# Kernel optimization log

Measured on AMD Instinct MI355X. Metric: run time of the kernel, lower is better.

## Reference

```python
import jax, jax.numpy as jnp
import numpy as np
from jax import lax

VOCAB, EMBED, CELL, LABELS = 32000, 128, 256, 128
B, T = 64, 256
N_LAYERS = 8


def _lstm_layer(x, mask, Wi, Wh, b, reverse):
    """Keras-semantics masked LSTM. x:[B,T,D], mask:[B,T] bool.
    If reverse (go_backwards=True): process reversed seq and return the
    REVERSED output sequence (Keras does NOT flip it back).
    Masked steps: carry h,c and emit previous h (Keras rnn mask behavior).
    Gate order i,f,c,o as in Keras kernels."""
    if reverse:
        x = x[:, ::-1]
        mask = mask[:, ::-1]
    Bs = x.shape[0]
    H = Wh.shape[0]
    xW = jnp.einsum('btd,dg->btg', x, Wi) + b  # [B,T,4H] precomputed input proj

    def step(carry, inp):
        h, c = carry
        g, m = inp  # g:[B,4H], m:[B]
        z = g + h @ Wh
        i, f, cb, o = jnp.split(z, 4, axis=-1)
        i = jax.nn.sigmoid(i)
        f = jax.nn.sigmoid(f)
        o = jax.nn.sigmoid(o)
        c_new = f * c + i * jnp.tanh(cb)
        h_new = o * jnp.tanh(c_new)
        m_ = m[:, None]
        h = jnp.where(m_, h_new, h)
        c = jnp.where(m_, c_new, c)
        return (h, c), h

    h0 = jnp.zeros((Bs, H), x.dtype)
    _, ys = lax.scan(step, (h0, h0), (xW.transpose(1, 0, 2), mask.T))
    return ys.transpose(1, 0, 2)  # [B,T,H], in processing order (no re-flip)


def setup_inputs() -> dict:
    key = jax.random.key(0)
    ks = jax.random.split(key, 9)
    word_ids = jax.random.randint(ks[0], (B, T), 0, VOCAB, dtype=jnp.int32)
    predicate_ids = jax.random.randint(ks[1], (B, T), 0, 2, dtype=jnp.int32)
    emb1 = jax.random.normal(ks[2], (VOCAB, EMBED), jnp.float32) * 0.1
    # binary feature embedding init: row0 zeros, row1 ones (as in source)
    emb2 = jnp.vstack([jnp.zeros((1, EMBED)), jnp.ones((1, EMBED))]).astype(jnp.float32)
    s = 0.05
    Wis = jax.random.normal(ks[3], (N_LAYERS, CELL, 4 * CELL), jnp.float32) * s  # layer0 in-dim 2*EMBED==CELL
    Whs = jax.random.normal(ks[4], (N_LAYERS, CELL, 4 * CELL), jnp.float32) * s
    bs = jnp.zeros((N_LAYERS, 4 * CELL), jnp.float32)
    bs = bs.at[:, CELL:2 * CELL].set(1.0)  # unit_forget_bias
    Wd = jax.random.normal(ks[5], (CELL, LABELS), jnp.float32) * s
    bd = jnp.zeros((LABELS,), jnp.float32)
    return {'word_ids': word_ids, 'predicate_ids': predicate_ids,
            'emb1': emb1, 'emb2': emb2, 'Wis': Wis, 'Whs': Whs, 'bs': bs,
            'Wd': Wd, 'bd': bd}


def reference(word_ids, predicate_ids, emb1, emb2, Wis, Whs, bs, Wd, bd):
    mask = word_ids != 0  # mask_zero semantics of embedding1
    encoded0 = jnp.concatenate([emb1[word_ids], emb2[predicate_ids]], axis=2)  # [B,T,2E]
    outs = []
    for i in range(N_LAYERS):
        if i == 0:
            inp = encoded0
        elif i == 1:
            inp = outs[0]
        else:
            inp = outs[i - 2] + outs[i - 1]
        outs.append(_lstm_layer(inp, mask, Wis[i], Whs[i], bs[i], reverse=(i % 2 == 1)))
    encoded_2d = (outs[6] + outs[7]).reshape(-1, CELL)  # [B*T, CELL]
    return jax.nn.softmax(encoded_2d @ Wd + bd, axis=-1)
```

## Files before the change

### kernel.cpp

```cpp
#include <hip/hip_runtime.h>


typedef _Float16 f16;
typedef _Float16 f16x8 __attribute__((ext_vector_type(8)));
typedef _Float16 f16x4 __attribute__((ext_vector_type(4)));
typedef float    f32x4 __attribute__((ext_vector_type(4)));

#define DEVI static __device__ __forceinline__

DEVI float fast_sigmoid(float x) {
  return __builtin_amdgcn_rcpf(1.f + __builtin_amdgcn_exp2f(-1.44269504f * x));
}
DEVI float fast_tanh(float x) {
  return 1.f - 2.f * __builtin_amdgcn_rcpf(1.f + __builtin_amdgcn_exp2f(2.88539008f * x));
}
DEVI int ntg_of(int w, int j2) { return ((j2 >> 1) << 4) + 2 * w + (j2 & 1); }

__global__ void pack_frags(const float* __restrict__ src, f16* __restrict__ dst, int nct) {
  const int idx  = blockIdx.x * 256 + threadIdx.x;
  const int lane = idx & 63;
  const int f    = idx >> 6;
  const int nt   = f % nct;
  const int g2   = f / nct;
  const int kk   = g2 & 7;
  const int L    = g2 >> 3;
  const int ncols = nct * 16;
  const float* s = src + (size_t)(L * 256 + kk * 32 + (lane >> 4) * 8) * ncols + nt * 16 + (lane & 15);
  f16x8 v;
#pragma unroll
  for (int e = 0; e < 8; ++e) v[e] = (f16)s[(size_t)e * ncols];
  *(f16x8*)(dst + (size_t)idx * 8) = v;
}

__global__ void embed_k(const int* __restrict__ wid, const int* __restrict__ pid,
                        const float* __restrict__ emb1, const float* __restrict__ emb2,
                        f16* __restrict__ X) {
  const int r = blockIdx.x;
  const int d = threadIdx.x;
  const int wv = wid[r], pv = pid[r];
  X[r * 256 + d]       = (f16)emb1[wv * 128 + d];
  X[r * 256 + 128 + d] = (f16)emb2[pv * 128 + d];
}

__global__ void make_input(const f16* __restrict__ a, const f16* __restrict__ b,
                           f16* __restrict__ X) {
  const size_t q = ((size_t)blockIdx.x * 256 + threadIdx.x) * 8;
  const f16x8 va = *(const f16x8*)(a + q);
  const f16x8 vb = *(const f16x8*)(b + q);
  *(f16x8*)(X + q) = va + vb;
}

__global__ __launch_bounds__(512, 2) void gemm_xw(const f16* __restrict__ X,
                                                  const f16* __restrict__ wipf,
                                                  const float* __restrict__ bias,
                                                  f16* __restrict__ xWp) {
  extern __shared__ char smem[];
  const int tid = threadIdx.x, lane = tid & 63, w = tid >> 6;
  const int nb = blockIdx.x, mb = blockIdx.y;
  const char* xbase = (const char*)X + (size_t)mb * 128 * 512;
#pragma unroll
  for (int i = 0; i < 8; ++i) {
    const int row = i * 16 + (tid >> 5);
    const int c16 = tid & 31;
    const uint4 v = *(const uint4*)(xbase + row * 512 + c16 * 16);
    *(uint4*)(smem + row * 512 + ((c16 ^ (row & 7)) << 4)) = v;
  }
  __syncthreads();

  const int mh = w >> 2, nw = w & 3;
  const char* wipf_c = (const char*)wipf;
  const float vb0 = bias[nb * 128 + nw * 32 + (lane & 15)];
  const float vb1 = bias[nb * 128 + nw * 32 + 16 + (lane & 15)];
  f32x4 acc[4][2] = {};
#pragma unroll
  for (int kk = 0; kk < 8; ++kk) {
    const f16x8 b0 = *(const f16x8*)(wipf_c + ((size_t)(kk * 64 + nb * 8 + nw * 2 + 0) << 10) + (lane << 4));
    const f16x8 b1 = *(const f16x8*)(wipf_c + ((size_t)(kk * 64 + nb * 8 + nw * 2 + 1) << 10) + (lane << 4));
#pragma unroll
    for (int m2 = 0; m2 < 4; ++m2) {
      const int row = mh * 64 + m2 * 16 + (lane & 15);
      const f16x8 a = *(const f16x8*)(smem + row * 512 + (((kk * 4 + (lane >> 4)) ^ (row & 7)) << 4));
      acc[m2][0] = __builtin_amdgcn_mfma_f32_16x16x32_f16(a, b0, acc[m2][0], 0, 0, 0);
      acc[m2][1] = __builtin_amdgcn_mfma_f32_16x16x32_f16(a, b1, acc[m2][1], 0, 0, 0);
    }
  }
#pragma unroll
  for (int m2 = 0; m2 < 4; ++m2)
#pragma unroll
    for (int n2 = 0; n2 < 2; ++n2)
#pragma unroll
      for (int j = 0; j < 4; ++j) {
        const int r   = mb * 128 + mh * 64 + m2 * 16 + (lane >> 4) * 4 + j;
        const int col = nb * 128 + nw * 32 + n2 * 16 + (lane & 15);
        xWp[(size_t)r * 1024 + (col & 255) * 4 + (col >> 8)] =
            (f16)(acc[m2][n2][j] + (n2 ? vb1 : vb0));
      }
}

__global__ __launch_bounds__(512, 2) void lstm_layer(
    const f16*  __restrict__ xWp,
    const int*  __restrict__ wid,
    const f16*  __restrict__ whp,
    f16* __restrict__ out,
    int reverse) {
  extern __shared__ char smem[];
  f16*      hbuf   = (f16*)(smem + 131072);
  unsigned* mask16 = (unsigned*)(smem + 147968);
  const int tid  = threadIdx.x;
  const int lane = tid & 63, w = tid >> 6;
  const int g    = blockIdx.x;
  const int r0   = lane & 15, rg = lane >> 4;
  const int ct0  = 2 * w;
  const char* whp_c = (const char*)whp;

  {
    const char* src = whp_c + (4 << 16);
#pragma unroll
    for (int i = 0; i < 16; ++i) {
      const int off = i * 8192 + tid * 16;
      *(uint4*)(smem + off) = *(const uint4*)(src + off);
    }
  }
  for (int i = tid; i < 2 * 16 * 264; i += 512) hbuf[i] = (f16)0.f;
  if (tid < 256) {
    unsigned m = 0;
#pragma unroll
    for (int j = 0; j < 16; ++j)
      m |= (wid[((g * 16 + j) << 8) + tid] != 0) ? (1u << j) : 0u;
    mask16[tid] = m;
  }

  f16x8 regB[32];
#pragma unroll
  for (int kk = 0; kk < 4; ++kk)
#pragma unroll
    for (int j2 = 0; j2 < 8; ++j2)
      regB[kk * 8 + j2] = *(const f16x8*)(whp_c + ((size_t)(kk * 64 + ntg_of(w, j2)) << 10) + (lane << 4));

  f16x8 sb6[8], sb7[8];
#pragma unroll
  for (int j2 = 0; j2 < 8; ++j2) {
    sb6[j2] = *(const f16x8*)(whp_c + ((size_t)(6 * 64 + ntg_of(w, j2)) << 10) + (lane << 4));
    sb7[j2] = *(const f16x8*)(whp_c + ((size_t)(7 * 64 + ntg_of(w, j2)) << 10) + (lane << 4));
  }

  float c[8], hreg[8];
#pragma unroll
  for (int i = 0; i < 8; ++i) { c[i] = 0.f; hreg[i] = 0.f; }

  __syncthreads();

#pragma unroll 1
  for (int k = 0; k < 256; ++k) {
    const int t_in = reverse ? (255 - k) : k;
    const f16* hc = hbuf + (k & 1) * 4224;
    f16*       hn = hbuf + ((k & 1) ^ 1) * 4224;

    f16x4 xwc[2][4];
#pragma unroll
    for (int p = 0; p < 2; ++p)
#pragma unroll
      for (int j = 0; j < 4; ++j)
        xwc[p][j] = *(const f16x4*)(xWp + (size_t)(((g * 16 + rg * 4 + j) << 8) + t_in) * 1024
                                    + ((ct0 + p) * 16 + r0) * 4);

    f32x4 acc[8] = {};
#pragma unroll
    for (int kk = 0; kk < 4; ++kk) {
      const f16x8 a = *(const f16x8*)&hc[r0 * 264 + kk * 32 + rg * 8];
#pragma unroll
      for (int j2 = 0; j2 < 8; ++j2)
        acc[j2] = __builtin_amdgcn_mfma_f32_16x16x32_f16(a, regB[kk * 8 + j2], acc[j2], 0, 0, 0);
    }

#pragma unroll
    for (int kk = 4; kk < 6; ++kk) {
      const f16x8 a = *(const f16x8*)&hc[r0 * 264 + kk * 32 + rg * 8];
#pragma unroll
      for (int j2 = 0; j2 < 8; ++j2) {
        const f16x8 b8 = *(const f16x8*)(smem + ((size_t)((kk - 4) * 64 + ntg_of(w, j2)) << 10) + (lane << 4));
        acc[j2] = __builtin_amdgcn_mfma_f32_16x16x32_f16(a, b8, acc[j2], 0, 0, 0);
      }
    }

    {
      const f16x8 a6 = *(const f16x8*)&hc[r0 * 264 + 6 * 32 + rg * 8];
#pragma unroll
      for (int j2 = 0; j2 < 8; ++j2)
        acc[j2] = __builtin_amdgcn_mfma_f32_16x16x32_f16(a6, sb6[j2], acc[j2], 0, 0, 0);
      const f16x8 a7 = *(const f16x8*)&hc[r0 * 264 + 7 * 32 + rg * 8];
#pragma unroll
      for (int j2 = 0; j2 < 8; ++j2)
        acc[j2] = __builtin_amdgcn_mfma_f32_16x16x32_f16(a7, sb7[j2], acc[j2], 0, 0, 0);
    }

    __builtin_amdgcn_sched_barrier(0);
#pragma unroll
    for (int j2 = 0; j2 < 8; ++j2) {
      sb6[j2] = *(const f16x8*)(whp_c + ((size_t)(6 * 64 + ntg_of(w, j2)) << 10) + (lane << 4));
      sb7[j2] = *(const f16x8*)(whp_c + ((size_t)(7 * 64 + ntg_of(w, j2)) << 10) + (lane << 4));
    }
    __builtin_amdgcn_sched_barrier(0);

    const unsigned mw = mask16[t_in];
#pragma unroll
    for (int p = 0; p < 2; ++p) {
#pragma unroll
      for (int j = 0; j < 4; ++j) {
        const int idx = p * 4 + j;
        const float zi = acc[0 + p][j] + (float)xwc[p][j][0];
        const float zf = acc[2 + p][j] + (float)xwc[p][j][1];
        const float zc = acc[4 + p][j] + (float)xwc[p][j][2];
        const float zo = acc[6 + p][j] + (float)xwc[p][j][3];
        const float ig = fast_sigmoid(zi);
        const float fg = fast_sigmoid(zf);
        const float og = fast_sigmoid(zo);
        const float cb = fast_tanh(zc);
        const float cn = fg * c[idx] + ig * cb;
        const float hv_ = og * fast_tanh(cn);
        const bool  m  = ((mw >> (rg * 4 + j)) & 1u) != 0u;
        c[idx]    = m ? cn : c[idx];
        hreg[idx] = m ? hv_ : hreg[idx];
      }
    }

#pragma unroll
    for (int p = 0; p < 2; ++p)
#pragma unroll
      for (int j = 0; j < 4; ++j) {
        const f16 hv = (f16)hreg[p * 4 + j];
        hn[(rg * 4 + j) * 264 + (ct0 + p) * 16 + r0] = hv;
        out[((size_t)((g * 16 + rg * 4 + j) << 8) + k) * 256 + (ct0 + p) * 16 + r0] = hv;
      }

    __builtin_amdgcn_sched_barrier(0);
    asm volatile("s_waitcnt lgkmcnt(0)\n\ts_barrier" ::: "memory");
    __builtin_amdgcn_sched_barrier(0);
  }
}

__global__ __launch_bounds__(512, 2) void final_k(const f16* __restrict__ o0,
                                                  const f16* __restrict__ o1,
                                                  const f16* __restrict__ wdpf,
                                                  const float* __restrict__ bd,
                                                  float* __restrict__ outp) {
  const int tid = threadIdx.x, lane = tid & 63, w = tid >> 6;
  const int rbase = blockIdx.x * 128 + w * 16;
  const char* wdpf_c = (const char*)wdpf;

  f32x4 acc[8] = {};
#pragma unroll
  for (int kk = 0; kk < 8; ++kk) {
    const int r  = rbase + (lane & 15);
    const int k0 = kk * 32 + (lane >> 4) * 8;
    const f16x8 x = *(const f16x8*)(o0 + (size_t)r * 256 + k0);
    const f16x8 y = *(const f16x8*)(o1 + (size_t)r * 256 + k0);
    const f16x8 a = x + y;
#pragma unroll
    for (int nt = 0; nt < 8; ++nt) {
      const f16x8 b = *(const f16x8*)(wdpf_c + ((size_t)(kk * 8 + nt) << 10) + (lane << 4));
      acc[nt] = __builtin_amdgcn_mfma_f32_16x16x32_f16(a, b, acc[nt], 0, 0, 0);
    }
  }

  float vb[8];
#pragma unroll
  for (int nt = 0; nt < 8; ++nt) vb[nt] = bd[nt * 16 + (lane & 15)];

#pragma unroll
  for (int j = 0; j < 4; ++j) {
    float v[8];
#pragma unroll
    for (int nt = 0; nt < 8; ++nt) v[nt] = acc[nt][j] + vb[nt];
    float mx = v[0];
#pragma unroll
    for (int nt = 1; nt < 8; ++nt) mx = fmaxf(mx, v[nt]);
#pragma unroll
    for (int m = 1; m < 16; m <<= 1) mx = fmaxf(mx, __shfl_xor(mx, m, 64));
    float s = 0.f;
#pragma unroll
    for (int nt = 0; nt < 8; ++nt) {
      v[nt] = __builtin_amdgcn_exp2f(1.44269504f * (v[nt] - mx));
      s += v[nt];
    }
#pragma unroll
    for (int m = 1; m < 16; m <<= 1) s += __shfl_xor(s, m, 64);
    const float rs = __builtin_amdgcn_rcpf(s);
    const int r = rbase + (lane >> 4) * 4 + j;
#pragma unroll
    for (int nt = 0; nt < 8; ++nt)
      outp[(size_t)r * 128 + nt * 16 + (lane & 15)] = v[nt] * rs;
  }
}

extern "C" void kernel_launch(void* const* d_in, const int* in_sizes, int n_in,
                              void* d_out, int out_size, void* d_ws, size_t ws_size,
                              hipStream_t stream) {
  const int*   wid  = (const int*)d_in[0];
  const int*   pid  = (const int*)d_in[1];
  const float* emb1 = (const float*)d_in[2];
  const float* emb2 = (const float*)d_in[3];
  const float* Wis  = (const float*)d_in[4];
  const float* Whs  = (const float*)d_in[5];
  const float* bs   = (const float*)d_in[6];
  const float* Wd   = (const float*)d_in[7];
  const float* bd   = (const float*)d_in[8];

  char* ws = (char*)d_ws;
  f16* Whp  = (f16*)(ws + 0);
  f16* Wipf = (f16*)(ws + 4194304);
  f16* Wdpf = (f16*)(ws + 8388608);
  f16* X    = (f16*)(ws + 8454144);
  f16* xWp  = (f16*)(ws + 16842752);
  f16* o0   = (f16*)(ws + 50397184);
  f16* o1   = (f16*)(ws + 58785792);

  hipFuncSetAttribute((const void*)gemm_xw,    hipFuncAttributeMaxDynamicSharedMemorySize, 65536);
  hipFuncSetAttribute((const void*)lstm_layer, hipFuncAttributeMaxDynamicSharedMemorySize, 148992);

  pack_frags<<<1024, 256, 0, stream>>>(Whs, Whp, 64);
  pack_frags<<<1024, 256, 0, stream>>>(Wis, Wipf, 64);
  pack_frags<<<16,   256, 0, stream>>>(Wd,  Wdpf, 8);
  embed_k<<<16384, 128, 0, stream>>>(wid, pid, emb1, emb2, X);

  f16* obuf[2] = {o0, o1};
  for (int L = 0; L < 8; ++L) {
    const f16* xin = X;
    if (L == 1) {
      xin = o0;
    } else if (L >= 2) {
      make_input<<<2048, 256, 0, stream>>>(obuf[L & 1], obuf[(L - 1) & 1], X);
    }
    gemm_xw<<<dim3(8, 128), 512, 65536, stream>>>(xin, Wipf + (size_t)L * 262144,
                                                  bs + L * 1024, xWp);
    lstm_layer<<<4, 512, 148992, stream>>>(xWp, wid, Whp + (size_t)L * 262144,
                                           obuf[L & 1], L & 1);
  }
  final_k<<<128, 512, 0, stream>>>(o0, o1, Wdpf, bd, (float*)d_out);
}
```

Measured before the change: 10.47 ms.

## Split LSTM recurrence across eight blocks with eight batch rows each

The recurrent LSTM kernel now runs 8 workgroups of 8 batch rows instead of 4 of 16, doubling the number of CUs working on the serial time loop. MFMA tiles still compute 16 rows, so half the rows are padding. Gate pre-activations are staged through an LDS z-buffer in two halves so each thread handles two columns of one row. This adds three extra barriers per timestep and uses a single h buffer instead of double buffering, trading more synchronisation and wasted MFMA work for more parallelism per step.

```diff
diff --git a/kernel.cpp b/kernel.cpp
--- a/kernel.cpp
+++ b/kernel.cpp
@@ -5,6 +5,7 @@
 typedef _Float16 f16x8 __attribute__((ext_vector_type(8)));
 typedef _Float16 f16x4 __attribute__((ext_vector_type(4)));
 typedef float    f32x4 __attribute__((ext_vector_type(4)));
+typedef float    f32x2 __attribute__((ext_vector_type(2)));
 
 #define DEVI static __device__ __forceinline__
 
@@ -104,14 +105,17 @@
     f16* __restrict__ out,
     int reverse) {
   extern __shared__ char smem[];
-  f16*      hbuf   = (f16*)(smem + 131072);
-  unsigned* mask16 = (unsigned*)(smem + 147968);
+  f16*      hbuf  = (f16*)(smem + 131072);
+  float*    zbuf  = (float*)(smem + 131072 + 8448);
+  unsigned* mask8 = (unsigned*)(smem + 131072 + 8448 + 16384);
   const int tid  = threadIdx.x;
   const int lane = tid & 63, w = tid >> 6;
   const int g    = blockIdx.x;
   const int r0   = lane & 15, rg = lane >> 4;
-  const int ct0  = 2 * w;
   const char* whp_c = (const char*)whp;
+  const int gr = w;
+  const int gc = lane * 2;
+  const size_t growbase = ((size_t)(g * 8 + gr)) << 8;
 
   {
     const char* src = whp_c + (4 << 16);
@@ -121,13 +125,13 @@
       *(uint4*)(smem + off) = *(const uint4*)(src + off);
     }
   }
-  for (int i = tid; i < 2 * 16 * 264; i += 512) hbuf[i] = (f16)0.f;
+  for (int i = tid; i < 16 * 264; i += 512) hbuf[i] = (f16)0.f;
   if (tid < 256) {
     unsigned m = 0;
 #pragma unroll
-    for (int j = 0; j < 16; ++j)
-      m |= (wid[((g * 16 + j) << 8) + tid] != 0) ? (1u << j) : 0u;
-    mask16[tid] = m;
+    for (int j = 0; j < 8; ++j)
+      m |= (wid[((g * 8 + j) << 8) + tid] != 0) ? (1u << j) : 0u;
+    mask8[tid] = m;
   }
 
   f16x8 regB[32];
@@ -144,51 +148,41 @@
     sb7[j2] = *(const f16x8*)(whp_c + ((size_t)(7 * 64 + ntg_of(w, j2)) << 10) + (lane << 4));
   }
 
-  float c[8], hreg[8];
-#pragma unroll
-  for (int i = 0; i < 8; ++i) { c[i] = 0.f; hreg[i] = 0.f; }
+  float c[4] = {0.f, 0.f, 0.f, 0.f}, hprev[4] = {0.f, 0.f, 0.f, 0.f};
 
   __syncthreads();
 
 #pragma unroll 1
   for (int k = 0; k < 256; ++k) {
     const int t_in = reverse ? (255 - k) : k;
-    const f16* hc = hbuf + (k & 1) * 4224;
-    f16*       hn = hbuf + ((k & 1) ^ 1) * 4224;
-
-    f16x4 xwc[2][4];
-#pragma unroll
-    for (int p = 0; p < 2; ++p)
-#pragma unroll
-      for (int j = 0; j < 4; ++j)
-        xwc[p][j] = *(const f16x4*)(xWp + (size_t)(((g * 16 + rg * 4 + j) << 8) + t_in) * 1024
-                                    + ((ct0 + p) * 16 + r0) * 4);
+
+    const f16* xrow = xWp + (growbase + t_in) * 1024;
+    const f16x8 xw0 = *(const f16x8*)(xrow + gc * 4);
+    const f16x8 xw1 = *(const f16x8*)(xrow + (128 + gc) * 4);
 
     f32x4 acc[8] = {};
 #pragma unroll
     for (int kk = 0; kk < 4; ++kk) {
-      const f16x8 a = *(const f16x8*)&hc[r0 * 264 + kk * 32 + rg * 8];
+      const f16x8 a = *(const f16x8*)&hbuf[r0 * 264 + kk * 32 + rg * 8];
 #pragma unroll
       for (int j2 = 0; j2 < 8; ++j2)
         acc[j2] = __builtin_amdgcn_mfma_f32_16x16x32_f16(a, regB[kk * 8 + j2], acc[j2], 0, 0, 0);
     }
-
 #pragma unroll
     for (int kk = 4; kk < 6; ++kk) {
-      const f16x8 a = *(const f16x8*)&hc[r0 * 264 + kk * 32 + rg * 8];
+      const f16x8 a = *(const f16x8*)&hbuf[r0 * 264 + kk * 32 + rg * 8];
 #pragma unroll
       for (int j2 = 0; j2 < 8; ++j2) {
         const f16x8 b8 = *(const f16x8*)(smem + ((size_t)((kk - 4) * 64 + ntg_of(w, j2)) << 10) + (lane << 4));
         acc[j2] = __builtin_amdgcn_mfma_f32_16x16x32_f16(a, b8, acc[j2], 0, 0, 0);
       }
     }
-
     {
-      const f16x8 a6 = *(const f16x8*)&hc[r0 * 264 + 6 * 32 + rg * 8];
+      const f16x8 a6 = *(const f16x8*)&hbuf[r0 * 264 + 6 * 32 + rg * 8];
 #pragma unroll
       for (int j2 = 0; j2 < 8; ++j2)
         acc[j2] = __builtin_amdgcn_mfma_f32_16x16x32_f16(a6, sb6[j2], acc[j2], 0, 0, 0);
-      const f16x8 a7 = *(const f16x8*)&hc[r0 * 264 + 7 * 32 + rg * 8];
+      const f16x8 a7 = *(const f16x8*)&hbuf[r0 * 264 + 7 * 32 + rg * 8];
 #pragma unroll
       for (int j2 = 0; j2 < 8; ++j2)
         acc[j2] = __builtin_amdgcn_mfma_f32_16x16x32_f16(a7, sb7[j2], acc[j2], 0, 0, 0);
@@ -202,37 +196,89 @@
     }
     __builtin_amdgcn_sched_barrier(0);
 
-    const unsigned mw = mask16[t_in];
-#pragma unroll
-    for (int p = 0; p < 2; ++p) {
-#pragma unroll
-      for (int j = 0; j < 4; ++j) {
-        const int idx = p * 4 + j;
-        const float zi = acc[0 + p][j] + (float)xwc[p][j][0];
-        const float zf = acc[2 + p][j] + (float)xwc[p][j][1];
-        const float zc = acc[4 + p][j] + (float)xwc[p][j][2];
-        const float zo = acc[6 + p][j] + (float)xwc[p][j][3];
+    const unsigned mw = mask8[t_in];
+    const bool mk = ((mw >> gr) & 1u) != 0u;
+
+    if (w < 4 && rg < 2) {
+#pragma unroll
+      for (int j2 = 0; j2 < 8; ++j2) {
+        const int q = j2 >> 1, p = j2 & 1;
+        const int col = (w & 3) * 32 + p * 16 + r0;
+#pragma unroll
+        for (int j = 0; j < 4; ++j)
+          zbuf[((rg * 4 + j) * 4 + q) * 128 + col] = acc[j2][j];
+      }
+    }
+    __builtin_amdgcn_sched_barrier(0);
+    asm volatile("s_waitcnt lgkmcnt(0)\n\ts_barrier" ::: "memory");
+    __builtin_amdgcn_sched_barrier(0);
+
+    {
+      f32x2 zq[4];
+#pragma unroll
+      for (int q = 0; q < 4; ++q)
+        zq[q] = *(const f32x2*)&zbuf[(gr * 4 + q) * 128 + gc];
+#pragma unroll
+      for (int jj = 0; jj < 2; ++jj) {
+        const float zi = zq[0][jj] + (float)xw0[jj * 4 + 0];
+        const float zf = zq[1][jj] + (float)xw0[jj * 4 + 1];
+        const float zc = zq[2][jj] + (float)xw0[jj * 4 + 2];
+        const float zo = zq[3][jj] + (float)xw0[jj * 4 + 3];
         const float ig = fast_sigmoid(zi);
         const float fg = fast_sigmoid(zf);
         const float og = fast_sigmoid(zo);
         const float cb = fast_tanh(zc);
-        const float cn = fg * c[idx] + ig * cb;
-        const float hv_ = og * fast_tanh(cn);
-        const bool  m  = ((mw >> (rg * 4 + j)) & 1u) != 0u;
-        c[idx]    = m ? cn : c[idx];
-        hreg[idx] = m ? hv_ : hreg[idx];
-      }
-    }
-
-#pragma unroll
-    for (int p = 0; p < 2; ++p)
-#pragma unroll
-      for (int j = 0; j < 4; ++j) {
-        const f16 hv = (f16)hreg[p * 4 + j];
-        hn[(rg * 4 + j) * 264 + (ct0 + p) * 16 + r0] = hv;
-        out[((size_t)((g * 16 + rg * 4 + j) << 8) + k) * 256 + (ct0 + p) * 16 + r0] = hv;
-      }
-
+        const float cn = fg * c[jj] + ig * cb;
+        const float hn = og * fast_tanh(cn);
+        c[jj]     = mk ? cn : c[jj];
+        hprev[jj] = mk ? hn : hprev[jj];
+        const f16 hv = (f16)hprev[jj];
+        hbuf[gr * 264 + gc + jj] = hv;
+        out[((growbase + k) << 8) + gc + jj] = hv;
+      }
+    }
+    __builtin_amdgcn_sched_barrier(0);
+    asm volatile("s_waitcnt lgkmcnt(0)\n\ts_barrier" ::: "memory");
+    __builtin_amdgcn_sched_barrier(0);
+
+    if (w >= 4 && rg < 2) {
+#pragma unroll
+      for (int j2 = 0; j2 < 8; ++j2) {
+        const int q = j2 >> 1, p = j2 & 1;
+        const int col = (w & 3) * 32 + p * 16 + r0;
+#pragma unroll
+        for (int j = 0; j < 4; ++j)
+          zbuf[((rg * 4 + j) * 4 + q) * 128 + col] = acc[j2][j];
+      }
+    }
+    __builtin_amdgcn_sched_barrier(0);
+    asm volatile("s_waitcnt lgkmcnt(0)\n\ts_barrier" ::: "memory");
+    __builtin_amdgcn_sched_barrier(0);
+
+    {
+      f32x2 zq[4];
+#pragma unroll
+      for (int q = 0; q < 4; ++q)
+        zq[q] = *(const f32x2*)&zbuf[(gr * 4 + q) * 128 + gc];
+#pragma unroll
+      for (int jj = 0; jj < 2; ++jj) {
+        const float zi = zq[0][jj] + (float)xw1[jj * 4 + 0];
+        const float zf = zq[1][jj] + (float)xw1[jj * 4 + 1];
+        const float zc = zq[2][jj] + (float)xw1[jj * 4 + 2];
+        const float zo = zq[3][jj] + (float)xw1[jj * 4 + 3];
+        const float ig = fast_sigmoid(zi);
+        const float fg = fast_sigmoid(zf);
+        const float og = fast_sigmoid(zo);
+        const float cb = fast_tanh(zc);
+        const float cn = fg * c[2 + jj] + ig * cb;
+        const float hn = og * fast_tanh(cn);
+        c[2 + jj]     = mk ? cn : c[2 + jj];
+        hprev[2 + jj] = mk ? hn : hprev[2 + jj];
+        const f16 hv = (f16)hprev[2 + jj];
+        hbuf[gr * 264 + 128 + gc + jj] = hv;
+        out[((growbase + k) << 8) + 128 + gc + jj] = hv;
+      }
+    }
     __builtin_amdgcn_sched_barrier(0);
     asm volatile("s_waitcnt lgkmcnt(0)\n\ts_barrier" ::: "memory");
     __builtin_amdgcn_sched_barrier(0);
@@ -316,7 +362,7 @@
   f16* o1   = (f16*)(ws + 58785792);
 
   hipFuncSetAttribute((const void*)gemm_xw,    hipFuncAttributeMaxDynamicSharedMemorySize, 65536);
-  hipFuncSetAttribute((const void*)lstm_layer, hipFuncAttributeMaxDynamicSharedMemorySize, 148992);
+  hipFuncSetAttribute((const void*)lstm_layer, hipFuncAttributeMaxDynamicSharedMemorySize, 156928);
 
   pack_frags<<<1024, 256, 0, stream>>>(Whs, Whp, 64);
   pack_frags<<<1024, 256, 0, stream>>>(Wis, Wipf, 64);
@@ -333,7 +379,7 @@
     }
     gemm_xw<<<dim3(8, 128), 512, 65536, stream>>>(xin, Wipf + (size_t)L * 262144,
                                                   bs + L * 1024, xWp);
-    lstm_layer<<<4, 512, 148992, stream>>>(xWp, wid, Whp + (size_t)L * 262144,
+    lstm_layer<<<8, 512, 156928, stream>>>(xWp, wid, Whp + (size_t)L * 262144,
                                            obuf[L & 1], L & 1);
   }
   final_k<<<128, 512, 0, stream>>>(o0, o1, Wdpf, bd, (float*)d_out);
```

Result: slower. 12.30 ms (+17.5%).

## Switch activations to time-major layout and pre-permute smem weight fragments

Applied to the files above, without the earlier changes.

Activation tensors (embeddings, xW projections, per-layer outputs) move from batch-major to time-major order. Each recurrent step then reads and writes one contiguous slab per timestep instead of rows strided by T. The recurrent weight fragments held in shared memory are reordered per wave so addressing becomes a simple base plus offset. The streamed sb6/sb7 global pointers are made wave-uniform with readfirstlane. The final kernel remaps rows back to batch-major for the output, which adds some index arithmetic and gathers in that kernel. The gemm_xw kernel is unchanged and relies on its row-agnostic handling.

```diff
diff --git a/kernel.cpp b/kernel.cpp
--- a/kernel.cpp
+++ b/kernel.cpp
@@ -15,6 +15,13 @@
   return 1.f - 2.f * __builtin_amdgcn_rcpf(1.f + __builtin_amdgcn_exp2f(2.88539008f * x));
 }
 DEVI int ntg_of(int w, int j2) { return ((j2 >> 1) << 4) + 2 * w + (j2 & 1); }
+
+DEVI const f16* upin(const f16* p) {
+  unsigned long long u = (unsigned long long)p;
+  unsigned lo = __builtin_amdgcn_readfirstlane((unsigned)u);
+  unsigned hi = __builtin_amdgcn_readfirstlane((unsigned)(u >> 32));
+  return (const f16*)(((unsigned long long)hi << 32) | lo);
+}
 
 __global__ void pack_frags(const float* __restrict__ src, f16* __restrict__ dst, int nct) {
   const int idx  = blockIdx.x * 256 + threadIdx.x;
@@ -35,11 +42,12 @@
 __global__ void embed_k(const int* __restrict__ wid, const int* __restrict__ pid,
                         const float* __restrict__ emb1, const float* __restrict__ emb2,
                         f16* __restrict__ X) {
-  const int r = blockIdx.x;
+  const int rix = blockIdx.x;
+  const int b = rix & 63, t = rix >> 6;
   const int d = threadIdx.x;
-  const int wv = wid[r], pv = pid[r];
-  X[r * 256 + d]       = (f16)emb1[wv * 128 + d];
-  X[r * 256 + 128 + d] = (f16)emb2[pv * 128 + d];
+  const int wv = wid[(b << 8) + t], pv = pid[(b << 8) + t];
+  X[rix * 256 + d]       = (f16)emb1[wv * 128 + d];
+  X[rix * 256 + 128 + d] = (f16)emb2[pv * 128 + d];
 }
 
 __global__ void make_input(const f16* __restrict__ a, const f16* __restrict__ b,
@@ -113,13 +121,14 @@
   const int ct0  = 2 * w;
   const char* whp_c = (const char*)whp;
 
-  {
-    const char* src = whp_c + (4 << 16);
-#pragma unroll
-    for (int i = 0; i < 16; ++i) {
-      const int off = i * 8192 + tid * 16;
-      *(uint4*)(smem + off) = *(const uint4*)(src + off);
-    }
+#pragma unroll
+  for (int i = 0; i < 16; ++i) {
+    const int idx  = tid + i * 512;
+    const int ln   = idx & 63, frag = idx >> 6;
+    const int wp   = frag >> 4, kkp = (frag >> 3) & 1, j2p = frag & 7;
+    const int nt   = ntg_of(wp, j2p);
+    *(uint4*)(smem + frag * 1024 + (ln << 4)) =
+        *(const uint4*)(whp_c + ((size_t)((4 + kkp) * 64 + nt) << 10) + (ln << 4));
   }
   for (int i = tid; i < 2 * 16 * 264; i += 512) hbuf[i] = (f16)0.f;
   if (tid < 256) {
@@ -137,12 +146,23 @@
     for (int j2 = 0; j2 < 8; ++j2)
       regB[kk * 8 + j2] = *(const f16x8*)(whp_c + ((size_t)(kk * 64 + ntg_of(w, j2)) << 10) + (lane << 4));
 
+  const f16* s6b[8];
+  const f16* s7b[8];
+#pragma unroll
+  for (int j2 = 0; j2 < 8; ++j2) {
+    s6b[j2] = upin(whp + ((size_t)(6 * 64 + ntg_of(w, j2)) << 9));
+    s7b[j2] = upin(whp + ((size_t)(7 * 64 + ntg_of(w, j2)) << 9));
+  }
+  const int lo8 = lane << 3;
+
   f16x8 sb6[8], sb7[8];
 #pragma unroll
   for (int j2 = 0; j2 < 8; ++j2) {
-    sb6[j2] = *(const f16x8*)(whp_c + ((size_t)(6 * 64 + ntg_of(w, j2)) << 10) + (lane << 4));
-    sb7[j2] = *(const f16x8*)(whp_c + ((size_t)(7 * 64 + ntg_of(w, j2)) << 10) + (lane << 4));
-  }
+    sb6[j2] = *(const f16x8*)(s6b[j2] + lo8);
+    sb7[j2] = *(const f16x8*)(s7b[j2] + lo8);
+  }
+
+  const char* wbase = smem + (w << 14) + (lane << 4);
 
   float c[8], hreg[8];
 #pragma unroll
@@ -156,12 +176,13 @@
     const f16* hc = hbuf + (k & 1) * 4224;
     f16*       hn = hbuf + ((k & 1) ^ 1) * 4224;
 
+    const f16* xk = xWp + ((size_t)t_in << 16);
     f16x4 xwc[2][4];
 #pragma unroll
     for (int p = 0; p < 2; ++p)
 #pragma unroll
       for (int j = 0; j < 4; ++j)
-        xwc[p][j] = *(const f16x4*)(xWp + (size_t)(((g * 16 + rg * 4 + j) << 8) + t_in) * 1024
+        xwc[p][j] = *(const f16x4*)(xk + (size_t)(g * 16 + rg * 4 + j) * 1024
                                     + ((ct0 + p) * 16 + r0) * 4);
 
     f32x4 acc[8] = {};
@@ -178,7 +199,7 @@
       const f16x8 a = *(const f16x8*)&hc[r0 * 264 + kk * 32 + rg * 8];
 #pragma unroll
       for (int j2 = 0; j2 < 8; ++j2) {
-        const f16x8 b8 = *(const f16x8*)(smem + ((size_t)((kk - 4) * 64 + ntg_of(w, j2)) << 10) + (lane << 4));
+        const f16x8 b8 = *(const f16x8*)(wbase + ((kk - 4) << 13) + (j2 << 10));
         acc[j2] = __builtin_amdgcn_mfma_f32_16x16x32_f16(a, b8, acc[j2], 0, 0, 0);
       }
     }
@@ -197,8 +218,8 @@
     __builtin_amdgcn_sched_barrier(0);
 #pragma unroll
     for (int j2 = 0; j2 < 8; ++j2) {
-      sb6[j2] = *(const f16x8*)(whp_c + ((size_t)(6 * 64 + ntg_of(w, j2)) << 10) + (lane << 4));
-      sb7[j2] = *(const f16x8*)(whp_c + ((size_t)(7 * 64 + ntg_of(w, j2)) << 10) + (lane << 4));
+      sb6[j2] = *(const f16x8*)(s6b[j2] + lo8);
+      sb7[j2] = *(const f16x8*)(s7b[j2] + lo8);
     }
     __builtin_amdgcn_sched_barrier(0);
 
@@ -224,13 +245,14 @@
       }
     }
 
+    f16* outk = out + ((size_t)k << 14) + (size_t)g * 4096;
 #pragma unroll
     for (int p = 0; p < 2; ++p)
 #pragma unroll
       for (int j = 0; j < 4; ++j) {
         const f16 hv = (f16)hreg[p * 4 + j];
         hn[(rg * 4 + j) * 264 + (ct0 + p) * 16 + r0] = hv;
-        out[((size_t)((g * 16 + rg * 4 + j) << 8) + k) * 256 + (ct0 + p) * 16 + r0] = hv;
+        outk[(rg * 4 + j) * 256 + (ct0 + p) * 16 + r0] = hv;
       }
 
     __builtin_amdgcn_sched_barrier(0);
@@ -248,13 +270,15 @@
   const int rbase = blockIdx.x * 128 + w * 16;
   const char* wdpf_c = (const char*)wdpf;
 
+  const int r   = rbase + (lane & 15);
+  const int rix = ((r & 255) << 6) + (r >> 8);
+
   f32x4 acc[8] = {};
 #pragma unroll
   for (int kk = 0; kk < 8; ++kk) {
-    const int r  = rbase + (lane & 15);
     const int k0 = kk * 32 + (lane >> 4) * 8;
-    const f16x8 x = *(const f16x8*)(o0 + (size_t)r * 256 + k0);
-    const f16x8 y = *(const f16x8*)(o1 + (size_t)r * 256 + k0);
+    const f16x8 x = *(const f16x8*)(o0 + (size_t)rix * 256 + k0);
+    const f16x8 y = *(const f16x8*)(o1 + (size_t)rix * 256 + k0);
     const f16x8 a = x + y;
 #pragma unroll
     for (int nt = 0; nt < 8; ++nt) {
@@ -286,10 +310,10 @@
 #pragma unroll
     for (int m = 1; m < 16; m <<= 1) s += __shfl_xor(s, m, 64);
     const float rs = __builtin_amdgcn_rcpf(s);
-    const int r = rbase + (lane >> 4) * 4 + j;
+    const int rr = rbase + (lane >> 4) * 4 + j;
 #pragma unroll
     for (int nt = 0; nt < 8; ++nt)
-      outp[(size_t)r * 128 + nt * 16 + (lane & 15)] = v[nt] * rs;
+      outp[(size_t)rr * 128 + nt * 16 + (lane & 15)] = v[nt] * rs;
   }
 }
 
```

After: 15.67 ms. +49.7%, slower.
